# Optimization experiments

Measured on AMD Instinct MI355X. Metric: run time of the kernel, lower is better.

Reference implementation:

```python
import jax, jax.numpy as jnp
import numpy as np

N_NODES = 500000
N_EDGES = 1250000
N_FEAT = 128
HIDDEN = 64
N_CLASSES = 10
N_GRAPHS = 512


def setup_inputs() -> dict:
    key = jax.random.key(0)
    ks = jax.random.split(key, 12)
    x = jax.random.normal(ks[0], (N_NODES, N_FEAT), dtype=jnp.float32)
    edge_index = jax.random.randint(ks[1], (2, N_EDGES), 0, N_NODES, dtype=jnp.int64)
    batch_index = jnp.sort(jax.random.randint(ks[2], (N_NODES,), 0, N_GRAPHS, dtype=jnp.int64))
    def glorot(k, fan_in, fan_out):
        s = jnp.sqrt(6.0 / (fan_in + fan_out))
        return jax.random.uniform(k, (fan_in, fan_out), jnp.float32, -s, s)
    return {
        "x": x,
        "edge_index": edge_index,
        "batch_index": batch_index,
        "W0": glorot(ks[3], N_FEAT, HIDDEN),
        "b0": jnp.zeros((HIDDEN,), jnp.float32),
        "W1": glorot(ks[4], HIDDEN, HIDDEN),
        "b1": jnp.zeros((HIDDEN,), jnp.float32),
        "W2": glorot(ks[5], HIDDEN, HIDDEN),
        "b2": jnp.zeros((HIDDEN,), jnp.float32),
        "Wout": glorot(ks[6], 2 * HIDDEN, N_CLASSES),
        "bout": jnp.zeros((N_CLASSES,), jnp.float32),
    }


def _gcn_norm(edge_index, n_nodes):
    # PyG GCNConv default: add self-loops, symmetric D^-1/2 (A+I) D^-1/2 norm.
    loop = jnp.arange(n_nodes, dtype=edge_index.dtype)
    src = jnp.concatenate([edge_index[0], loop])  # message sources
    dst = jnp.concatenate([edge_index[1], loop])  # aggregation targets
    deg = jax.ops.segment_sum(jnp.ones_like(dst, dtype=jnp.float32), dst,
                              num_segments=n_nodes)
    dinv = jnp.where(deg > 0, jax.lax.rsqrt(deg), 0.0)
    norm = dinv[src] * dinv[dst]  # [E+N]
    return src, dst, norm


def _gcn_conv(h, W, b, src, dst, norm, n_nodes):
    h = h @ W  # transform first (PyG applies lin before propagate)
    msg = h[src] * norm[:, None]  # gather + scale, [E+N, C]
    out = jax.ops.segment_sum(msg, dst, num_segments=n_nodes)
    return out + b


def reference(x, edge_index, batch_index, W0, b0, W1, b1, W2, b2, Wout, bout):
    n = x.shape[0]
    src, dst, norm = _gcn_norm(edge_index, n)
    h = jax.nn.relu(_gcn_conv(x, W0, b0, src, dst, norm, n))
    h = jax.nn.relu(_gcn_conv(h, W1, b1, src, dst, norm, n))
    h = jax.nn.relu(_gcn_conv(h, W2, b2, src, dst, norm, n))
    # global mean / max pool over graphs
    gsum = jax.ops.segment_sum(h, batch_index, num_segments=N_GRAPHS)
    cnt = jax.ops.segment_sum(jnp.ones((n,), jnp.float32), batch_index,
                              num_segments=N_GRAPHS)
    gmean = gsum / jnp.maximum(cnt, 1.0)[:, None]
    gmax = jax.ops.segment_max(h, batch_index, num_segments=N_GRAPHS)
    gmax = jnp.where(jnp.isneginf(gmax), 0.0, gmax)  # guard empty graphs
    pooled = jnp.concatenate([gmean, gmax], axis=1)  # [G, 2H]
    return pooled @ Wout + bout
```

## Files before the change

kernel.cpp:

```cpp
#include <hip/hip_runtime.h>
#include <hip/hip_bf16.h>

#define NN 500000
#define NE 1250000
#define NF 128
#define NH 64
#define NC 10
#define NG 512
#define ELLW 8

typedef __attribute__((ext_vector_type(8))) short short8;
typedef __attribute__((ext_vector_type(4))) float floatx4;

__device__ __forceinline__ unsigned short f2bf(float f) {
  unsigned u = __builtin_bit_cast(unsigned, f);
  u += 0x7FFFu + ((u >> 16) & 1u);
  return (unsigned short)(u >> 16);
}
__device__ __forceinline__ float bf2f(unsigned short u) {
  return __builtin_bit_cast(float, (unsigned)u << 16);
}
__device__ __forceinline__ float asf(int i) { return __builtin_bit_cast(float, i); }

__device__ __forceinline__ void fma8(float acc[8], float n, short8 v) {
#pragma unroll
  for (int k = 0; k < 8; ++k) acc[k] = fmaf(n, bf2f((unsigned short)v[k]), acc[k]);
}

__global__ __launch_bounds__(256) void k_init(int* __restrict__ deg, int* __restrict__ cur,
                                              int* __restrict__ counter,
                                              float* __restrict__ gsum, int* __restrict__ gmax,
                                              int* __restrict__ gcnt,
                                              int4* __restrict__ ell4,
                                              const float* __restrict__ W0,
                                              const float* __restrict__ W1,
                                              const float* __restrict__ W2,
                                              unsigned short* __restrict__ Wt0,
                                              unsigned short* __restrict__ Wt1,
                                              unsigned short* __restrict__ Wt2) {
  int i = blockIdx.x * 256 + threadIdx.x;
  if (i < NN) {
    deg[i] = 0; cur[i] = 0;
    int4 p; p.x = i; p.y = 0; p.z = i; p.w = 0;
    ell4[(size_t)i * 4 + 0] = p;
    ell4[(size_t)i * 4 + 1] = p;
    ell4[(size_t)i * 4 + 2] = p;
    ell4[(size_t)i * 4 + 3] = p;
  }
  if (i == 0) *counter = 0;
  if (i < NG * 64) { gsum[i] = 0.f; gmax[i] = 0; }
  if (i < NG) gcnt[i] = 0;
  if (i < NF * 64) { int k = i / 64, n = i % 64; Wt0[n * NF + k] = f2bf(W0[i]); }
  if (i < 64 * 64) {
    int k = i / 64, n = i % 64;
    Wt1[n * 64 + k] = f2bf(W1[i]);
    Wt2[n * 64 + k] = f2bf(W2[i]);
  }
}

__global__ __launch_bounds__(256) void k_deg(const int* __restrict__ dst, int* __restrict__ deg) {
  int e = blockIdx.x * 256 + threadIdx.x;
  if (e < NE) atomicAdd(&deg[dst[e]], 1);
}

__global__ __launch_bounds__(256) void k_dinv_rs(const int* __restrict__ deg,
                                                 float* __restrict__ dinv,
                                                 int* __restrict__ row_start,
                                                 int* __restrict__ counter) {
  int i = blockIdx.x * 256 + threadIdx.x;
  int lane = threadIdx.x & 63;
  int d = 0;
  if (i < NN) {
    d = deg[i];
    dinv[i] = rsqrtf((float)(d + 1));
  }
  int od = d > ELLW ? d - ELLW : 0;
  int incl = od;
#pragma unroll
  for (int off = 1; off < 64; off <<= 1) {
    int n = __shfl_up(incl, off, 64);
    if (lane >= off) incl += n;
  }
  int total = __shfl(incl, 63, 64);
  int base = 0;
  if (lane == 63) base = atomicAdd(counter, total);
  base = __shfl(base, 63, 64);
  if (i < NN) row_start[i] = base + incl - od;
}

__global__ __launch_bounds__(256) void k_fill(const int* __restrict__ ei,
                                              const float* __restrict__ dinv,
                                              int* __restrict__ cur,
                                              int2* __restrict__ ell,
                                              const int* __restrict__ ostart,
                                              int2* __restrict__ ovf) {
  int e = blockIdx.x * 256 + threadIdx.x;
  if (e >= NE) return;
  int s = ei[e];
  int d = ei[NE + e];
  float nrm = dinv[s] * dinv[d];
  int slot = atomicAdd(&cur[d], 1);
  int2 v;
  v.x = s;
  v.y = __builtin_bit_cast(int, nrm);
  if (slot < ELLW) ell[(size_t)d * ELLW + slot] = v;
  else ovf[ostart[d] + slot - ELLW] = v;
}

__global__ __launch_bounds__(256) void k_gemm_f32(const float* __restrict__ Ain,
                                                  const unsigned short* __restrict__ Wt,
                                                  unsigned short* __restrict__ linbf) {
  constexpr int K = 128, KC = 4, SP = K + 8;
  __shared__ unsigned short Wl[64 * SP];
  int tid = threadIdx.x;
  for (int idx = tid * 8; idx < 64 * K; idx += 2048) {
    int n = idx / K, k = idx % K;
    *(short8*)&Wl[n * SP + k] = *(const short8*)&Wt[idx];
  }
  __syncthreads();

  int lane = tid & 63, wave = tid >> 6;
  int quad = lane >> 4, l16 = lane & 15;

  short8 bfrag[4][KC];
#pragma unroll
  for (int nt = 0; nt < 4; ++nt)
#pragma unroll
    for (int kc = 0; kc < KC; ++kc)
      bfrag[nt][kc] = *(const short8*)&Wl[(nt * 16 + l16) * SP + kc * 32 + quad * 8];

  const int ntiles = NN / 16;
  for (int t0 = (blockIdx.x * 4 + wave) * 2; t0 < ntiles; t0 += gridDim.x * 8) {
    floatx4 acc[2][4];
    floatx4 araw[2][KC][2];
#pragma unroll
    for (int tt = 0; tt < 2; ++tt) {
      int arow = (t0 + tt) * 16 + l16;
      const float* Ab = Ain + (size_t)arow * K + quad * 8;
#pragma unroll
      for (int kc = 0; kc < KC; ++kc) {
        araw[tt][kc][0] = *(const floatx4*)(Ab + kc * 32);
        araw[tt][kc][1] = *(const floatx4*)(Ab + kc * 32 + 4);
      }
    }
#pragma unroll
    for (int tt = 0; tt < 2; ++tt) {
      floatx4 z = {0.f, 0.f, 0.f, 0.f};
#pragma unroll
      for (int nt = 0; nt < 4; ++nt) acc[tt][nt] = z;
#pragma unroll
      for (int kc = 0; kc < KC; ++kc) {
        short8 af;
#pragma unroll
        for (int q = 0; q < 4; ++q) {
          af[q] = (short)f2bf(araw[tt][kc][0][q]);
          af[q + 4] = (short)f2bf(araw[tt][kc][1][q]);
        }
#pragma unroll
        for (int nt = 0; nt < 4; ++nt)
          acc[tt][nt] = __builtin_amdgcn_mfma_f32_16x16x32_bf16(af, bfrag[nt][kc], acc[tt][nt], 0, 0, 0);
      }
#pragma unroll
      for (int i = 0; i < 4; ++i) {
        int r = (t0 + tt) * 16 + quad * 4 + i;
        unsigned short* lp = linbf + (size_t)r * 64 + l16;
#pragma unroll
        for (int nt = 0; nt < 4; ++nt) lp[nt * 16] = f2bf(acc[tt][nt][i]);
      }
    }
  }
}

__global__ __launch_bounds__(256) void k_agg(const unsigned short* __restrict__ linbf,
                                             const float* __restrict__ dinv,
                                             const float* __restrict__ bias,
                                             const int* __restrict__ deg,
                                             const int2* __restrict__ ell,
                                             const int* __restrict__ ostart,
                                             const int2* __restrict__ ovf,
                                             unsigned short* __restrict__ hout) {
  int tid = threadIdx.x;
  int lane = tid & 63, wave = tid >> 6;
  int g = lane >> 3, sl = lane & 7, fb = sl * 8;
  int r = blockIdx.x * 32 + wave * 8 + g;

  const int4* ellv = (const int4*)(ell + (size_t)r * ELLW);
  int4 q0 = ellv[0], q1 = ellv[1], q2 = ellv[2], q3 = ellv[3];
  int dg = deg[r];
  float dv = dinv[r];
  short8 hs = *(const short8*)&linbf[(size_t)r * 64 + fb];
  short8 g0 = *(const short8*)&linbf[(size_t)q0.x * 64 + fb];
  short8 g1 = *(const short8*)&linbf[(size_t)q0.z * 64 + fb];
  short8 g2 = *(const short8*)&linbf[(size_t)q1.x * 64 + fb];
  short8 g3 = *(const short8*)&linbf[(size_t)q1.z * 64 + fb];
  float acc[8];
  float sw = dv * dv;
#pragma unroll
  for (int k = 0; k < 8; ++k) acc[k] = bf2f((unsigned short)hs[k]) * sw;
  fma8(acc, asf(q0.y), g0);
  fma8(acc, asf(q0.w), g1);
  fma8(acc, asf(q1.y), g2);
  fma8(acc, asf(q1.w), g3);
  if (dg > 4) {
    short8 g4 = *(const short8*)&linbf[(size_t)q2.x * 64 + fb];
    short8 g5 = *(const short8*)&linbf[(size_t)q2.z * 64 + fb];
    short8 g6 = *(const short8*)&linbf[(size_t)q3.x * 64 + fb];
    short8 g7 = *(const short8*)&linbf[(size_t)q3.z * 64 + fb];
    fma8(acc, asf(q2.y), g4);
    fma8(acc, asf(q2.w), g5);
    fma8(acc, asf(q3.y), g6);
    fma8(acc, asf(q3.w), g7);
  }
  if (dg > ELLW) {
    int rs = ostart[r], on = dg - ELLW;
    for (int j = 0; j < on; j += 2) {
      int2 e0 = ovf[rs + j];
      int2 e1 = ovf[rs + j + 1];
      int rem = on - j;
      int sx1 = rem > 1 ? e1.x : r;
      float n1 = rem > 1 ? asf(e1.y) : 0.f;
      short8 f0 = *(const short8*)&linbf[(size_t)e0.x * 64 + fb];
      short8 f1 = *(const short8*)&linbf[(size_t)sx1 * 64 + fb];
      fma8(acc, asf(e0.y), f0);
      fma8(acc, n1, f1);
    }
  }
  floatx4 bv0 = *(const floatx4*)&bias[fb];
  floatx4 bv1 = *(const floatx4*)&bias[fb + 4];
  short8 o;
#pragma unroll
  for (int k = 0; k < 8; ++k) {
    float bk = k < 4 ? bv0[k] : bv1[k - 4];
    o[k] = (short)f2bf(fmaxf(acc[k] + bk, 0.f));
  }
  *(short8*)&hout[(size_t)r * 64 + fb] = o;
}

template <int POOL>
__global__ __launch_bounds__(256) void k_layer(const unsigned short* __restrict__ hin,
                                               const float* __restrict__ dinv,
                                               const float* __restrict__ bias,
                                               const int* __restrict__ deg,
                                               const int2* __restrict__ ell,
                                               const int* __restrict__ ostart,
                                               const int2* __restrict__ ovf,
                                               const unsigned short* __restrict__ Wt,
                                               unsigned short* __restrict__ hout,
                                               float* __restrict__ gsum,
                                               int* __restrict__ gmax,
                                               int* __restrict__ gcnt,
                                               const int* __restrict__ batch) {
  constexpr int SP = 72;
  constexpr int SLDS = POOL ? (64 * 66 * 2) : (64 * SP);
  __shared__ unsigned short Wl[64 * 64];
  __shared__ unsigned short Sl[SLDS];
  float* smemf = (float*)Sl;
  int tid = threadIdx.x;
  int lane = tid & 63, wave = tid >> 6, quad = lane >> 4, l16 = lane & 15;
  int g = lane >> 3, sl = lane & 7, fb = sl * 8;

  for (int idx = tid * 8; idx < 64 * 64; idx += 2048)
    *(short8*)&Wl[idx] = *(const short8*)&Wt[idx];

  float bb[4];
#pragma unroll
  for (int nt = 0; nt < 4; ++nt) bb[nt] = bias[nt * 16 + l16];

  int base = blockIdx.x * 64;

#pragma unroll
  for (int it = 0; it < 2; ++it) {
    int row = wave * 16 + it * 8 + g;
    int r = base + row;
    int rr = r < NN ? r : NN - 1;
    const int4* ellv = (const int4*)(ell + (size_t)rr * ELLW);
    int4 q0 = ellv[0], q1 = ellv[1], q2 = ellv[2], q3 = ellv[3];
    int dg = deg[rr];
    float dv = dinv[rr];
    short8 hs = *(const short8*)&hin[(size_t)rr * 64 + fb];
    short8 g0 = *(const short8*)&hin[(size_t)q0.x * 64 + fb];
    short8 g1 = *(const short8*)&hin[(size_t)q0.z * 64 + fb];
    short8 g2 = *(const short8*)&hin[(size_t)q1.x * 64 + fb];
    short8 g3 = *(const short8*)&hin[(size_t)q1.z * 64 + fb];
    float acc[8];
    float sw = dv * dv;
#pragma unroll
    for (int k = 0; k < 8; ++k) acc[k] = bf2f((unsigned short)hs[k]) * sw;
    fma8(acc, asf(q0.y), g0);
    fma8(acc, asf(q0.w), g1);
    fma8(acc, asf(q1.y), g2);
    fma8(acc, asf(q1.w), g3);
    if (dg > 4) {
      short8 g4 = *(const short8*)&hin[(size_t)q2.x * 64 + fb];
      short8 g5 = *(const short8*)&hin[(size_t)q2.z * 64 + fb];
      short8 g6 = *(const short8*)&hin[(size_t)q3.x * 64 + fb];
      short8 g7 = *(const short8*)&hin[(size_t)q3.z * 64 + fb];
      fma8(acc, asf(q2.y), g4);
      fma8(acc, asf(q2.w), g5);
      fma8(acc, asf(q3.y), g6);
      fma8(acc, asf(q3.w), g7);
    }
    if (dg > ELLW) {
      int rs = ostart[rr], on = dg - ELLW;
      for (int j = 0; j < on; j += 2) {
        int2 e0 = ovf[rs + j];
        int2 e1 = ovf[rs + j + 1];
        int rem = on - j;
        int sx1 = rem > 1 ? e1.x : rr;
        float n1 = rem > 1 ? asf(e1.y) : 0.f;
        short8 f0 = *(const short8*)&hin[(size_t)e0.x * 64 + fb];
        short8 f1 = *(const short8*)&hin[(size_t)sx1 * 64 + fb];
        fma8(acc, asf(e0.y), f0);
        fma8(acc, n1, f1);
      }
    }
    short8 o;
#pragma unroll
    for (int k = 0; k < 8; ++k) o[k] = (short)f2bf(acc[k]);
    *(short8*)&Sl[row * SP + fb] = o;
  }

  __syncthreads();

  short8 bfrag[4][2];
#pragma unroll
  for (int nt = 0; nt < 4; ++nt)
#pragma unroll
    for (int kc = 0; kc < 2; ++kc)
      bfrag[nt][kc] = *(const short8*)&Wl[(nt * 16 + l16) * 64 + kc * 32 + quad * 8];

  floatx4 z = {0.f, 0.f, 0.f, 0.f};
  floatx4 acc4[4] = {z, z, z, z};
#pragma unroll
  for (int kc = 0; kc < 2; ++kc) {
    short8 af = *(const short8*)&Sl[(wave * 16 + l16) * SP + kc * 32 + quad * 8];
#pragma unroll
    for (int nt = 0; nt < 4; ++nt)
      acc4[nt] = __builtin_amdgcn_mfma_f32_16x16x32_bf16(af, bfrag[nt][kc], acc4[nt], 0, 0, 0);
  }

  if constexpr (!POOL) {
#pragma unroll
    for (int i = 0; i < 4; ++i) {
      int r = base + wave * 16 + quad * 4 + i;
      if (r < NN) {
        unsigned short* hp = hout + (size_t)r * 64 + l16;
#pragma unroll
        for (int nt = 0; nt < 4; ++nt)
          hp[nt * 16] = f2bf(fmaxf(acc4[nt][i] + bb[nt], 0.f));
      }
    }
  } else {
    __shared__ int sb[64];
    __shared__ float reds[256];
    __shared__ float redm[256];
    __shared__ int redc[4];
    __syncthreads();
#pragma unroll
    for (int i = 0; i < 4; ++i) {
      int row = wave * 16 + quad * 4 + i;
#pragma unroll
      for (int nt = 0; nt < 4; ++nt)
        smemf[row * 66 + nt * 16 + l16] = fmaxf(acc4[nt][i] + bb[nt], 0.f);
    }
    if (tid < 64) sb[tid] = (base + tid < NN) ? batch[base + tid] : 0x7fffffff;
    __syncthreads();
    int nvalid = NN - base; if (nvalid > 64) nvalid = 64;
    int gs = sb[0], ge = sb[nvalid - 1];
    int feat = tid & 63, strip = tid >> 6;
    for (int gg = gs; gg <= ge; ++gg) {
      float s = 0.f, m = 0.f;
      int cl = 0;
#pragma unroll
      for (int j = 0; j < 16; ++j) {
        int row = strip * 16 + j;
        float v = smemf[row * 66 + feat];
        if (sb[row] == gg) { s += v; m = fmaxf(m, v); cl++; }
      }
      reds[tid] = s;
      redm[tid] = m;
      if (feat == 0) redc[strip] = cl;
      __syncthreads();
      if (strip == 0) {
        s += reds[64 + feat] + reds[128 + feat] + reds[192 + feat];
        m = fmaxf(fmaxf(m, redm[64 + feat]), fmaxf(redm[128 + feat], redm[192 + feat]));
        atomicAdd(&gsum[gg * 64 + feat], s);
        atomicMax(&gmax[gg * 64 + feat], __builtin_bit_cast(int, m));
        if (feat == 0) atomicAdd(&gcnt[gg], redc[0] + redc[1] + redc[2] + redc[3]);
      }
      __syncthreads();
    }
  }
}

__global__ __launch_bounds__(128) void k_head(const float* __restrict__ gsum,
                                              const int* __restrict__ gmax,
                                              const int* __restrict__ gcnt,
                                              const float* __restrict__ Wout,
                                              const float* __restrict__ bout,
                                              float* __restrict__ out) {
  __shared__ float p[128];
  int g = blockIdx.x, tid = threadIdx.x;
  if (tid < 64) {
    int c = gcnt[g];
    float inv = c > 0 ? 1.0f / (float)c : 0.f;
    p[tid] = gsum[g * 64 + tid] * inv;
    p[64 + tid] = asf(gmax[g * 64 + tid]);
  }
  __syncthreads();
  if (tid < NC) {
    float acc = bout[tid];
#pragma unroll 8
    for (int c2 = 0; c2 < 128; ++c2) acc += p[c2] * Wout[c2 * NC + tid];
    out[g * NC + tid] = acc;
  }
}

extern "C" void kernel_launch(void* const* d_in, const int* in_sizes, int n_in,
                              void* d_out, int out_size, void* d_ws, size_t ws_size,
                              hipStream_t stream) {
  const float* x     = (const float*)d_in[0];
  const int*   ei    = (const int*)d_in[1];
  const int*   batch = (const int*)d_in[2];
  const float* W0    = (const float*)d_in[3];
  const float* b0    = (const float*)d_in[4];
  const float* W1    = (const float*)d_in[5];
  const float* b1    = (const float*)d_in[6];
  const float* W2    = (const float*)d_in[7];
  const float* b2    = (const float*)d_in[8];
  const float* Wout  = (const float*)d_in[9];
  const float* bout  = (const float*)d_in[10];
  float* out = (float*)d_out;

  char* ws = (char*)d_ws;
  size_t off = 0;
  auto alloc = [&](size_t bytes) -> void* {
    void* p = ws + off;
    off = (off + bytes + 255) & ~(size_t)255;
    return p;
  };
  int*   deg     = (int*)alloc((size_t)NN * 4);
  int*   counter = (int*)alloc(4);
  float* dinv    = (float*)alloc((size_t)NN * 4);
  int*   ostart  = (int*)alloc((size_t)NN * 4);
  int*   cur     = (int*)alloc((size_t)NN * 4);
  int2*  ell     = (int2*)alloc((size_t)NN * ELLW * 8);
  int2*  ovf     = (int2*)alloc(((size_t)NE + 4) * 8);
  unsigned short* linbf = (unsigned short*)alloc((size_t)NN * 64 * 2);
  unsigned short* H1    = (unsigned short*)alloc((size_t)NN * 64 * 2);
  unsigned short* H2    = (unsigned short*)alloc((size_t)NN * 64 * 2);
  unsigned short* Wt0 = (unsigned short*)alloc(64 * 128 * 2);
  unsigned short* Wt1 = (unsigned short*)alloc(64 * 64 * 2);
  unsigned short* Wt2 = (unsigned short*)alloc(64 * 64 * 2);
  float* gsum = (float*)alloc((size_t)NG * 64 * 4);
  int*   gmax = (int*)alloc((size_t)NG * 64 * 4);
  int*   gcnt = (int*)alloc((size_t)NG * 4);

  k_init<<<(NN + 255) / 256, 256, 0, stream>>>(deg, cur, counter, gsum, gmax, gcnt,
                                               (int4*)ell, W0, W1, W2, Wt0, Wt1, Wt2);
  k_deg<<<(NE + 255) / 256, 256, 0, stream>>>(ei + NE, deg);
  k_dinv_rs<<<(NN + 255) / 256, 256, 0, stream>>>(deg, dinv, ostart, counter);
  k_fill<<<(NE + 255) / 256, 256, 0, stream>>>(ei, dinv, cur, ell, ostart, ovf);

  k_gemm_f32<<<2048, 256, 0, stream>>>(x, Wt0, linbf);
  k_agg<<<NN / 32, 256, 0, stream>>>(linbf, dinv, b0, deg, ell, ostart, ovf, H1);
  k_layer<0><<<(NN + 63) / 64, 256, 0, stream>>>(H1, dinv, b1, deg, ell, ostart, ovf, Wt1, H2,
                                                 nullptr, nullptr, nullptr, nullptr);
  k_layer<1><<<(NN + 63) / 64, 256, 0, stream>>>(H2, dinv, b2, deg, ell, ostart, ovf, Wt2, nullptr,
                                                 gsum, gmax, gcnt, batch);
  k_head<<<NG, 128, 0, stream>>>(gsum, gmax, gcnt, Wout, bout, out);
}
```

Baseline: 775.9 us.

## Stage per-row ELL metadata in LDS and drop block barrier in layer kernels

In the aggregation and layer kernels, each wave now loads its 16 rows of ELL entries, degree, dinv and overflow start into shared memory with one coalesced load per lane. This replaces the redundant per-lane global loads that were issued for every row. The layer kernel no longer stages the weight matrix in LDS, and it drops the __syncthreads, because each wave only reads the Sl rows it wrote itself. MFMA weight fragments now come straight from global memory instead. k_agg now processes 64 rows per block, two rows per thread, with bounds guards. This relies on wave-local ordering of the LDS accesses, and it trades LDS reuse of the weights for more global and L2 reads.

```diff
diff --git a/kernel.cpp b/kernel.cpp
--- a/kernel.cpp
+++ b/kernel.cpp
@@ -179,61 +179,84 @@
                                              const int* __restrict__ ostart,
                                              const int2* __restrict__ ovf,
                                              unsigned short* __restrict__ hout) {
+  __shared__ int4  mell[256];
+  __shared__ int   mdeg[64];
+  __shared__ float mdinv[64];
+  __shared__ int   mos[64];
   int tid = threadIdx.x;
   int lane = tid & 63, wave = tid >> 6;
   int g = lane >> 3, sl = lane & 7, fb = sl * 8;
-  int r = blockIdx.x * 32 + wave * 8 + g;
-
-  const int4* ellv = (const int4*)(ell + (size_t)r * ELLW);
-  int4 q0 = ellv[0], q1 = ellv[1], q2 = ellv[2], q3 = ellv[3];
-  int dg = deg[r];
-  float dv = dinv[r];
-  short8 hs = *(const short8*)&linbf[(size_t)r * 64 + fb];
-  short8 g0 = *(const short8*)&linbf[(size_t)q0.x * 64 + fb];
-  short8 g1 = *(const short8*)&linbf[(size_t)q0.z * 64 + fb];
-  short8 g2 = *(const short8*)&linbf[(size_t)q1.x * 64 + fb];
-  short8 g3 = *(const short8*)&linbf[(size_t)q1.z * 64 + fb];
-  float acc[8];
-  float sw = dv * dv;
-#pragma unroll
-  for (int k = 0; k < 8; ++k) acc[k] = bf2f((unsigned short)hs[k]) * sw;
-  fma8(acc, asf(q0.y), g0);
-  fma8(acc, asf(q0.w), g1);
-  fma8(acc, asf(q1.y), g2);
-  fma8(acc, asf(q1.w), g3);
-  if (dg > 4) {
-    short8 g4 = *(const short8*)&linbf[(size_t)q2.x * 64 + fb];
-    short8 g5 = *(const short8*)&linbf[(size_t)q2.z * 64 + fb];
-    short8 g6 = *(const short8*)&linbf[(size_t)q3.x * 64 + fb];
-    short8 g7 = *(const short8*)&linbf[(size_t)q3.z * 64 + fb];
-    fma8(acc, asf(q2.y), g4);
-    fma8(acc, asf(q2.w), g5);
-    fma8(acc, asf(q3.y), g6);
-    fma8(acc, asf(q3.w), g7);
-  }
-  if (dg > ELLW) {
-    int rs = ostart[r], on = dg - ELLW;
-    for (int j = 0; j < on; j += 2) {
-      int2 e0 = ovf[rs + j];
-      int2 e1 = ovf[rs + j + 1];
-      int rem = on - j;
-      int sx1 = rem > 1 ? e1.x : r;
-      float n1 = rem > 1 ? asf(e1.y) : 0.f;
-      short8 f0 = *(const short8*)&linbf[(size_t)e0.x * 64 + fb];
-      short8 f1 = *(const short8*)&linbf[(size_t)sx1 * 64 + fb];
-      fma8(acc, asf(e0.y), f0);
-      fma8(acc, n1, f1);
-    }
-  }
-  floatx4 bv0 = *(const floatx4*)&bias[fb];
-  floatx4 bv1 = *(const floatx4*)&bias[fb + 4];
-  short8 o;
-#pragma unroll
-  for (int k = 0; k < 8; ++k) {
-    float bk = k < 4 ? bv0[k] : bv1[k - 4];
-    o[k] = (short)f2bf(fmaxf(acc[k] + bk, 0.f));
-  }
-  *(short8*)&hout[(size_t)r * 64 + fb] = o;
+  int base = blockIdx.x * 64;
+
+  {
+    int nr = base + wave * 16 + (lane >> 2);
+    int nc = nr < NN ? nr : NN - 1;
+    mell[wave * 64 + lane] = ((const int4*)ell)[(size_t)nc * 4 + (lane & 3)];
+    int nr2 = base + wave * 16 + (lane & 15);
+    int nc2 = nr2 < NN ? nr2 : NN - 1;
+    if (lane < 16)      mdeg[wave * 16 + lane]         = deg[nc2];
+    else if (lane < 32) mdinv[wave * 16 + (lane - 16)] = dinv[nc2];
+    else if (lane < 48) mos[wave * 16 + (lane - 32)]   = ostart[nc2];
+  }
+
+#pragma unroll
+  for (int it = 0; it < 2; ++it) {
+    int row = wave * 16 + it * 8 + g;
+    int r = base + row;
+    int rr = r < NN ? r : NN - 1;
+    int4 q0 = mell[row * 4 + 0], q1 = mell[row * 4 + 1];
+    int4 q2 = mell[row * 4 + 2], q3 = mell[row * 4 + 3];
+    int dg = mdeg[row];
+    float dv = mdinv[row];
+    short8 hs = *(const short8*)&linbf[(size_t)rr * 64 + fb];
+    short8 g0 = *(const short8*)&linbf[(size_t)q0.x * 64 + fb];
+    short8 g1 = *(const short8*)&linbf[(size_t)q0.z * 64 + fb];
+    short8 g2 = *(const short8*)&linbf[(size_t)q1.x * 64 + fb];
+    short8 g3 = *(const short8*)&linbf[(size_t)q1.z * 64 + fb];
+    float acc[8];
+    float sw = dv * dv;
+#pragma unroll
+    for (int k = 0; k < 8; ++k) acc[k] = bf2f((unsigned short)hs[k]) * sw;
+    fma8(acc, asf(q0.y), g0);
+    fma8(acc, asf(q0.w), g1);
+    fma8(acc, asf(q1.y), g2);
+    fma8(acc, asf(q1.w), g3);
+    if (dg > 4) {
+      short8 g4 = *(const short8*)&linbf[(size_t)q2.x * 64 + fb];
+      short8 g5 = *(const short8*)&linbf[(size_t)q2.z * 64 + fb];
+      short8 g6 = *(const short8*)&linbf[(size_t)q3.x * 64 + fb];
+      short8 g7 = *(const short8*)&linbf[(size_t)q3.z * 64 + fb];
+      fma8(acc, asf(q2.y), g4);
+      fma8(acc, asf(q2.w), g5);
+      fma8(acc, asf(q3.y), g6);
+      fma8(acc, asf(q3.w), g7);
+    }
+    if (dg > ELLW) {
+      int rs = mos[row], on = dg - ELLW;
+      for (int j = 0; j < on; j += 2) {
+        int2 e0 = ovf[rs + j];
+        int2 e1 = ovf[rs + j + 1];
+        int rem = on - j;
+        int sx1 = rem > 1 ? e1.x : rr;
+        float n1 = rem > 1 ? asf(e1.y) : 0.f;
+        short8 f0 = *(const short8*)&linbf[(size_t)e0.x * 64 + fb];
+        short8 f1 = *(const short8*)&linbf[(size_t)sx1 * 64 + fb];
+        fma8(acc, asf(e0.y), f0);
+        fma8(acc, n1, f1);
+      }
+    }
+    if (r < NN) {
+      floatx4 bv0 = *(const floatx4*)&bias[fb];
+      floatx4 bv1 = *(const floatx4*)&bias[fb + 4];
+      short8 o;
+#pragma unroll
+      for (int k = 0; k < 8; ++k) {
+        float bk = k < 4 ? bv0[k] : bv1[k - 4];
+        o[k] = (short)f2bf(fmaxf(acc[k] + bk, 0.f));
+      }
+      *(short8*)&hout[(size_t)r * 64 + fb] = o;
+    }
+  }
 }
 
 template <int POOL>
@@ -252,31 +275,37 @@
                                                const int* __restrict__ batch) {
   constexpr int SP = 72;
   constexpr int SLDS = POOL ? (64 * 66 * 2) : (64 * SP);
-  __shared__ unsigned short Wl[64 * 64];
   __shared__ unsigned short Sl[SLDS];
+  __shared__ int4  mell[256];
+  __shared__ int   mdeg[64];
+  __shared__ float mdinv[64];
+  __shared__ int   mos[64];
   float* smemf = (float*)Sl;
   int tid = threadIdx.x;
   int lane = tid & 63, wave = tid >> 6, quad = lane >> 4, l16 = lane & 15;
   int g = lane >> 3, sl = lane & 7, fb = sl * 8;
-
-  for (int idx = tid * 8; idx < 64 * 64; idx += 2048)
-    *(short8*)&Wl[idx] = *(const short8*)&Wt[idx];
-
-  float bb[4];
-#pragma unroll
-  for (int nt = 0; nt < 4; ++nt) bb[nt] = bias[nt * 16 + l16];
-
   int base = blockIdx.x * 64;
+
+  {
+    int nr = base + wave * 16 + (lane >> 2);
+    int nc = nr < NN ? nr : NN - 1;
+    mell[wave * 64 + lane] = ((const int4*)ell)[(size_t)nc * 4 + (lane & 3)];
+    int nr2 = base + wave * 16 + (lane & 15);
+    int nc2 = nr2 < NN ? nr2 : NN - 1;
+    if (lane < 16)      mdeg[wave * 16 + lane]         = deg[nc2];
+    else if (lane < 32) mdinv[wave * 16 + (lane - 16)] = dinv[nc2];
+    else if (lane < 48) mos[wave * 16 + (lane - 32)]   = ostart[nc2];
+  }
 
 #pragma unroll
   for (int it = 0; it < 2; ++it) {
     int row = wave * 16 + it * 8 + g;
     int r = base + row;
     int rr = r < NN ? r : NN - 1;
-    const int4* ellv = (const int4*)(ell + (size_t)rr * ELLW);
-    int4 q0 = ellv[0], q1 = ellv[1], q2 = ellv[2], q3 = ellv[3];
-    int dg = deg[rr];
-    float dv = dinv[rr];
+    int4 q0 = mell[row * 4 + 0], q1 = mell[row * 4 + 1];
+    int4 q2 = mell[row * 4 + 2], q3 = mell[row * 4 + 3];
+    int dg = mdeg[row];
+    float dv = mdinv[row];
     short8 hs = *(const short8*)&hin[(size_t)rr * 64 + fb];
     short8 g0 = *(const short8*)&hin[(size_t)q0.x * 64 + fb];
     short8 g1 = *(const short8*)&hin[(size_t)q0.z * 64 + fb];
@@ -301,11 +330,11 @@
       fma8(acc, asf(q3.w), g7);
     }
     if (dg > ELLW) {
-      int rs = ostart[rr], on = dg - ELLW;
-      for (int j = 0; j < on; j += 2) {
-        int2 e0 = ovf[rs + j];
-        int2 e1 = ovf[rs + j + 1];
-        int rem = on - j;
+      int rs = mos[row], on = dg - ELLW;
+      for (int jj = 0; jj < on; jj += 2) {
+        int2 e0 = ovf[rs + jj];
+        int2 e1 = ovf[rs + jj + 1];
+        int rem = on - jj;
         int sx1 = rem > 1 ? e1.x : rr;
         float n1 = rem > 1 ? asf(e1.y) : 0.f;
         short8 f0 = *(const short8*)&hin[(size_t)e0.x * 64 + fb];
@@ -320,14 +349,15 @@
     *(short8*)&Sl[row * SP + fb] = o;
   }
 
-  __syncthreads();
-
   short8 bfrag[4][2];
 #pragma unroll
   for (int nt = 0; nt < 4; ++nt)
 #pragma unroll
     for (int kc = 0; kc < 2; ++kc)
-      bfrag[nt][kc] = *(const short8*)&Wl[(nt * 16 + l16) * 64 + kc * 32 + quad * 8];
+      bfrag[nt][kc] = *(const short8*)&Wt[(nt * 16 + l16) * 64 + kc * 32 + quad * 8];
+  float bb[4];
+#pragma unroll
+  for (int nt = 0; nt < 4; ++nt) bb[nt] = bias[nt * 16 + l16];
 
   floatx4 z = {0.f, 0.f, 0.f, 0.f};
   floatx4 acc4[4] = {z, z, z, z};
@@ -463,7 +493,7 @@
   k_fill<<<(NE + 255) / 256, 256, 0, stream>>>(ei, dinv, cur, ell, ostart, ovf);
 
   k_gemm_f32<<<2048, 256, 0, stream>>>(x, Wt0, linbf);
-  k_agg<<<NN / 32, 256, 0, stream>>>(linbf, dinv, b0, deg, ell, ostart, ovf, H1);
+  k_agg<<<(NN + 63) / 64, 256, 0, stream>>>(linbf, dinv, b0, deg, ell, ostart, ovf, H1);
   k_layer<0><<<(NN + 63) / 64, 256, 0, stream>>>(H1, dinv, b1, deg, ell, ostart, ovf, Wt1, H2,
                                                  nullptr, nullptr, nullptr, nullptr);
   k_layer<1><<<(NN + 63) / 64, 256, 0, stream>>>(H2, dinv, b2, deg, ell, ostart, ovf, Wt2, nullptr,
```

New measurement: 782.7 us. Within noise of the previous version (+0.9%).
